# Optimization experiments

Hardware: AMD Instinct MI355X
Metric: run time of the kernel (lower is better)

## Reference

```python
import jax, jax.numpy as jnp
import numpy as np

N_QUBITS = 4
N_LAYERS = 2
BATCH = 524288


def _apply_1q(state, U, axis):
    # state: [B, 2,2,2,2]; U: [2,2] (shared) or [B,2,2] (per-sample); axis = wire index + 1
    s = jnp.moveaxis(state, axis, -1)
    if U.ndim == 3:
        s = jnp.einsum('bij,b...j->b...i', U, s)
    else:
        s = jnp.einsum('ij,...j->...i', U, s)
    return jnp.moveaxis(s, -1, axis)


def _apply_cz(state, a, b):
    # diagonal CZ: flip sign where both qubits are |1>
    sign = jnp.array([[1.0, 1.0], [1.0, -1.0]], dtype=state.dtype)
    shape = [1] * state.ndim
    shape[a] = 2
    shape[b] = 2
    return state * sign.reshape(shape)


def _quantum_expval(feats, w):
    # feats: [B, n_qubits] angles; w: [n_layers, n_qubits, 3] Rot params
    B = feats.shape[0]
    state = jnp.zeros((B,) + (2,) * N_QUBITS, jnp.complex64)
    state = state.at[(slice(None),) + (0,) * N_QUBITS].set(1.0)
    # per-sample RY embedding
    for i in range(N_QUBITS):
        c = jnp.cos(feats[:, i] * 0.5)
        s = jnp.sin(feats[:, i] * 0.5)
        U = jnp.stack([jnp.stack([c, -s], -1), jnp.stack([s, c], -1)], -2).astype(jnp.complex64)
        state = _apply_1q(state, U, i + 1)
    # variational layers: Rot(phi,theta,omega) = RZ(omega) RY(theta) RZ(phi), then CZ chain
    for l in range(N_LAYERS):
        for i in range(N_QUBITS):
            phi, theta, omega = w[l, i, 0], w[l, i, 1], w[l, i, 2]
            ct = jnp.cos(theta * 0.5)
            st = jnp.sin(theta * 0.5)
            U = jnp.stack([
                jnp.stack([jnp.exp(-0.5j * (phi + omega)) * ct, -jnp.exp(0.5j * (phi - omega)) * st]),
                jnp.stack([jnp.exp(-0.5j * (phi - omega)) * st, jnp.exp(0.5j * (phi + omega)) * ct]),
            ]).astype(jnp.complex64)
            state = _apply_1q(state, U, i + 1)
        for i in range(N_QUBITS - 1):
            state = _apply_cz(state, i + 1, i + 2)
    probs = jnp.square(jnp.abs(state))
    p = probs.sum(axis=tuple(range(2, N_QUBITS + 1)))  # marginal of wire 0 -> [B, 2]
    return (p[:, 0] - p[:, 1]).astype(jnp.float32)  # <Z_0>


def setup_inputs() -> dict:
    key = jax.random.key(0)
    ks = jax.random.split(key, 12)
    f = jnp.float32
    return {
        'text': jax.random.normal(ks[0], (BATCH, 16), f),
        'image': jax.random.normal(ks[1], (BATCH, 48), f),
        'tW1': jax.random.normal(ks[2], (16, 32), f) * 0.25,
        'tb1': jnp.zeros((32,), f),
        'tW2': jax.random.normal(ks[3], (32, N_QUBITS), f) * 0.18,
        'tb2': jnp.zeros((N_QUBITS,), f),
        'iW1': jax.random.normal(ks[4], (48, 64), f) * 0.14,
        'ib1': jnp.zeros((64,), f),
        'iW2': jax.random.normal(ks[5], (64, N_QUBITS), f) * 0.125,
        'ib2': jnp.zeros((N_QUBITS,), f),
        'qweights': jax.random.normal(ks[6], (N_LAYERS, N_QUBITS, 3), f),
        'cW1': jax.random.normal(ks[7], (1, 16), f),
        'cb1': jnp.zeros((16,), f),
        'cW2': jax.random.normal(ks[8], (16, 2), f) * 0.25,
        'cb2': jnp.zeros((2,), f),
    }


def reference(text, image, tW1, tb1, tW2, tb2, iW1, ib1, iW2, ib2, qweights, cW1, cb1, cW2, cb2):
    tf = jax.nn.relu(text @ tW1 + tb1) @ tW2 + tb2      # [B, 4]
    imf = jax.nn.relu(image @ iW1 + ib1) @ iW2 + ib2    # [B, 4]
    feats = (tf + imf) * 0.5                             # [B, 4]
    q = _quantum_expval(feats, qweights)                 # [B]
    h = jax.nn.relu(q[:, None] @ cW1 + cb1)              # [B, 16]
    return h @ cW2 + cb2                                 # [B, 2]
```

## Files before the change

kernel.cpp:

```cpp
#include <hip/hip_runtime.h>
#include <math.h>

#define NQ 4
#define NL 2

__global__ void qnn_precompute_A(const float* __restrict__ qw, float* __restrict__ A)
{
    __shared__ float Mre[16][16];
    __shared__ float Mim[16][16];
    int t = threadIdx.x;
    if (t < 16) {
        int j = t;
        float re[16], im[16];
        for (int b = 0; b < 16; ++b) { re[b] = (b == j) ? 1.f : 0.f; im[b] = 0.f; }
        for (int l = 0; l < NL; ++l) {
            for (int i = 0; i < NQ; ++i) {
                float phi   = qw[(l*NQ + i)*3 + 0];
                float theta = qw[(l*NQ + i)*3 + 1];
                float omega = qw[(l*NQ + i)*3 + 2];
                float ct, st; sincosf(0.5f*theta, &st, &ct);
                float ap = 0.5f*(phi + omega);
                float am = 0.5f*(phi - omega);
                float cap, sap, cam, sam;
                sincosf(ap, &sap, &cap);
                sincosf(am, &sam, &cam);
                float u00r =  cap*ct, u00i = -sap*ct;
                float u01r = -cam*st, u01i = -sam*st;
                float u10r =  cam*st, u10i = -sam*st;
                float u11r =  cap*ct, u11i =  sap*ct;
                int mask = 1 << (3 - i);
                for (int b = 0; b < 16; ++b) {
                    if (b & mask) continue;
                    int b1 = b | mask;
                    float a0r = re[b],  a0i = im[b];
                    float a1r = re[b1], a1i = im[b1];
                    re[b]  = u00r*a0r - u00i*a0i + u01r*a1r - u01i*a1i;
                    im[b]  = u00r*a0i + u00i*a0r + u01r*a1i + u01i*a1r;
                    re[b1] = u10r*a0r - u10i*a0i + u11r*a1r - u11i*a1i;
                    im[b1] = u10r*a0i + u10i*a0r + u11r*a1i + u11i*a1r;
                }
            }
            for (int b = 0; b < 16; ++b) {
                float sgn = 1.f;
                if ((b & 0xC) == 0xC) sgn = -sgn;
                if ((b & 0x6) == 0x6) sgn = -sgn;
                if ((b & 0x3) == 0x3) sgn = -sgn;
                re[b] *= sgn; im[b] *= sgn;
            }
        }
        for (int b = 0; b < 16; ++b) { Mre[j][b] = re[b]; Mim[j][b] = im[b]; }
    }
    __syncthreads();
    {
        int j = t >> 4, k = t & 15;
        float s = 0.f;
        #pragma unroll
        for (int b = 0; b < 16; ++b) {
            float sg = (b & 8) ? -1.f : 1.f;
            s += sg * (Mre[j][b]*Mre[k][b] + Mim[j][b]*Mim[k][b]);
        }
        A[j*16 + k] = s;
    }
}

__global__ __launch_bounds__(256, 4) void qnn_main(
    const float* __restrict__ text, const float* __restrict__ image,
    const float* __restrict__ tW1, const float* __restrict__ tb1,
    const float* __restrict__ tW2, const float* __restrict__ tb2,
    const float* __restrict__ iW1, const float* __restrict__ ib1,
    const float* __restrict__ iW2, const float* __restrict__ ib2,
    const float* __restrict__ A,
    const float* __restrict__ cW1, const float* __restrict__ cb1,
    const float* __restrict__ cW2, const float* __restrict__ cb2,
    float* __restrict__ out, int B)
{
    int b = blockIdx.x * blockDim.x + threadIdx.x;
    if (b >= B) return;

    float h2[64];
    #pragma unroll
    for (int j = 0; j < 64; ++j) h2[j] = ib1[j];
    {
        const float4* i4 = (const float4*)(image + (size_t)b * 48);
        #pragma unroll 2
        for (int k4 = 0; k4 < 12; ++k4) {
            float4 v = i4[k4];
            const float* w = iW1 + k4 * 4 * 64;
            #pragma unroll
            for (int j = 0; j < 64; ++j) h2[j] = fmaf(v.x, w[j],       h2[j]);
            #pragma unroll
            for (int j = 0; j < 64; ++j) h2[j] = fmaf(v.y, w[64 + j],  h2[j]);
            #pragma unroll
            for (int j = 0; j < 64; ++j) h2[j] = fmaf(v.z, w[128 + j], h2[j]);
            #pragma unroll
            for (int j = 0; j < 64; ++j) h2[j] = fmaf(v.w, w[192 + j], h2[j]);
        }
    }
    float imf[4];
    #pragma unroll
    for (int o = 0; o < 4; ++o) imf[o] = ib2[o];
    #pragma unroll
    for (int j = 0; j < 64; ++j) {
        float r = fmaxf(h2[j], 0.f);
        const float* w2 = iW2 + j * 4;
        #pragma unroll
        for (int o = 0; o < 4; ++o) imf[o] = fmaf(r, w2[o], imf[o]);
    }

    float h1[32];
    #pragma unroll
    for (int j = 0; j < 32; ++j) h1[j] = tb1[j];
    {
        const float4* t4 = (const float4*)(text + (size_t)b * 16);
        #pragma unroll
        for (int k4 = 0; k4 < 4; ++k4) {
            float4 v = t4[k4];
            const float* w = tW1 + k4 * 4 * 32;
            #pragma unroll
            for (int j = 0; j < 32; ++j) h1[j] = fmaf(v.x, w[j],      h1[j]);
            #pragma unroll
            for (int j = 0; j < 32; ++j) h1[j] = fmaf(v.y, w[32 + j], h1[j]);
            #pragma unroll
            for (int j = 0; j < 32; ++j) h1[j] = fmaf(v.z, w[64 + j], h1[j]);
            #pragma unroll
            for (int j = 0; j < 32; ++j) h1[j] = fmaf(v.w, w[96 + j], h1[j]);
        }
    }
    float tf[4];
    #pragma unroll
    for (int o = 0; o < 4; ++o) tf[o] = tb2[o];
    #pragma unroll
    for (int j = 0; j < 32; ++j) {
        float r = fmaxf(h1[j], 0.f);
        const float* w2 = tW2 + j * 4;
        #pragma unroll
        for (int o = 0; o < 4; ++o) tf[o] = fmaf(r, w2[o], tf[o]);
    }

    float c[4], s[4];
    #pragma unroll
    for (int i = 0; i < 4; ++i) {
        float f = (tf[i] + imf[i]) * 0.25f;
        __sincosf(f, &s[i], &c[i]);
    }
    float p01[4] = { c[0]*c[1], c[0]*s[1], s[0]*c[1], s[0]*s[1] };
    float p23[4] = { c[2]*c[3], c[2]*s[3], s[2]*c[3], s[2]*s[3] };
    float psi[16];
    #pragma unroll
    for (int x = 0; x < 4; ++x)
        #pragma unroll
        for (int y = 0; y < 4; ++y)
            psi[x*4+y] = p01[x] * p23[y];

    float q = 0.f;
    #pragma unroll
    for (int j = 0; j < 16; ++j) {
        float row = 0.f;
        #pragma unroll
        for (int k = 0; k < 16; ++k) row = fmaf(A[j*16+k], psi[k], row);
        q = fmaf(psi[j], row, q);
    }

    float o0 = cb2[0], o1 = cb2[1];
    #pragma unroll
    for (int j = 0; j < 16; ++j) {
        float h = fmaxf(fmaf(q, cW1[j], cb1[j]), 0.f);
        o0 = fmaf(h, cW2[j*2+0], o0);
        o1 = fmaf(h, cW2[j*2+1], o1);
    }
    float2* o2 = (float2*)out;
    o2[b] = make_float2(o0, o1);
}

extern "C" void kernel_launch(void* const* d_in, const int* in_sizes, int n_in,
                              void* d_out, int out_size, void* d_ws, size_t ws_size,
                              hipStream_t stream)
{
    const float* text  = (const float*)d_in[0];
    const float* image = (const float*)d_in[1];
    const float* tW1   = (const float*)d_in[2];
    const float* tb1   = (const float*)d_in[3];
    const float* tW2   = (const float*)d_in[4];
    const float* tb2   = (const float*)d_in[5];
    const float* iW1   = (const float*)d_in[6];
    const float* ib1   = (const float*)d_in[7];
    const float* iW2   = (const float*)d_in[8];
    const float* ib2   = (const float*)d_in[9];
    const float* qw    = (const float*)d_in[10];
    const float* cW1   = (const float*)d_in[11];
    const float* cb1   = (const float*)d_in[12];
    const float* cW2   = (const float*)d_in[13];
    const float* cb2   = (const float*)d_in[14];

    float* A = (float*)d_ws;
    int B = in_sizes[0] / 16;

    qnn_precompute_A<<<1, 256, 0, stream>>>(qw, A);

    int block = 256;
    int grid = (B + block - 1) / block;
    qnn_main<<<grid, block, 0, stream>>>(
        text, image, tW1, tb1, tW2, tb2, iW1, ib1, iW2, ib2,
        A, cW1, cb1, cW2, cb2, (float*)d_out, B);
}
```

Measured before the change: 257.6 us.

## Fuse A precompute into main kernel, stage weights in LDS, 4 samples per thread with packed FMA

Merges the separate A-matrix precompute kernel into one fused kernel in which every block recomputes A and stages all MLP weights in shared memory. Each thread now handles four samples, using 2-wide float vectors so the compiler can emit packed FMA, and the hidden layer is processed in 16-wide chunks to limit register pressure. This reuses each weight read across four samples and removes a kernel launch. In exchange every block pays for weight staging and the redundant A computation, and occupancy changes because of the larger LDS footprint and the new launch bounds.

```diff
diff --git a/kernel.cpp b/kernel.cpp
--- a/kernel.cpp
+++ b/kernel.cpp
@@ -4,31 +4,91 @@
 #define NQ 4
 #define NL 2
 
-__global__ void qnn_precompute_A(const float* __restrict__ qw, float* __restrict__ A)
+typedef float v2f __attribute__((ext_vector_type(2)));
+
+static __device__ __forceinline__ v2f vsplat(float x) { v2f r; r.x = x; r.y = x; return r; }
+static __device__ __forceinline__ v2f vfma(v2f a, float b, v2f c) {
+#if __has_builtin(__builtin_elementwise_fma)
+    return __builtin_elementwise_fma(a, vsplat(b), c);
+#else
+    v2f r; r.x = __builtin_fmaf(a.x, b, c.x); r.y = __builtin_fmaf(a.y, b, c.y); return r;
+#endif
+}
+static __device__ __forceinline__ v2f vfmav(v2f a, v2f b, v2f c) {
+#if __has_builtin(__builtin_elementwise_fma)
+    return __builtin_elementwise_fma(a, b, c);
+#else
+    v2f r; r.x = __builtin_fmaf(a.x, b.x, c.x); r.y = __builtin_fmaf(a.y, b.y, c.y); return r;
+#endif
+}
+static __device__ __forceinline__ v2f vrelu(v2f a) {
+    v2f r; r.x = fmaxf(a.x, 0.f); r.y = fmaxf(a.y, 0.f); return r;
+}
+static __device__ __forceinline__ float fget(float4 v, int k) {
+    return (k == 0) ? v.x : (k == 1) ? v.y : (k == 2) ? v.z : v.w;
+}
+
+#define O_IW1 0
+#define O_IW2 3072
+#define O_TW1 3328
+#define O_TW2 3840
+#define O_IB1 3968
+#define O_TB1 4032
+#define O_FB2 4064
+#define O_CW1 4068
+#define O_CB1 4084
+#define O_CW2 4100
+#define O_CB2 4132
+#define O_AS  4136
+#define O_MRE 4392
+#define O_MIM 4648
+#define LDS_FLOATS 4904
+
+__global__ __launch_bounds__(256, 3) void qnn_fused(
+    const float* __restrict__ text, const float* __restrict__ image,
+    const float* __restrict__ tW1, const float* __restrict__ tb1,
+    const float* __restrict__ tW2, const float* __restrict__ tb2,
+    const float* __restrict__ iW1, const float* __restrict__ ib1,
+    const float* __restrict__ iW2, const float* __restrict__ ib2,
+    const float* __restrict__ qw,
+    const float* __restrict__ cW1, const float* __restrict__ cb1,
+    const float* __restrict__ cW2, const float* __restrict__ cb2,
+    float* __restrict__ out, int B)
 {
-    __shared__ float Mre[16][16];
-    __shared__ float Mim[16][16];
-    int t = threadIdx.x;
-    if (t < 16) {
-        int j = t;
+    __shared__ __align__(16) float W[LDS_FLOATS];
+    const int tid = threadIdx.x;
+
+    for (int i = tid; i < 3072; i += 256) W[O_IW1 + i] = iW1[i];
+    W[O_IW2 + tid] = iW2[tid];
+    for (int i = tid; i < 512; i += 256) W[O_TW1 + i] = tW1[i];
+    if (tid < 128) W[O_TW2 + tid] = tW2[tid];
+    if (tid < 64)  W[O_IB1 + tid] = ib1[tid];
+    if (tid < 32)  W[O_TB1 + tid] = tb1[tid];
+    if (tid < 4)   W[O_FB2 + tid] = ib2[tid] + tb2[tid];
+    if (tid < 16) { W[O_CW1 + tid] = cW1[tid]; W[O_CB1 + tid] = cb1[tid]; }
+    if (tid < 32)  W[O_CW2 + tid] = cW2[tid];
+    if (tid < 2)   W[O_CB2 + tid] = cb2[tid];
+
+    if (tid < 16) {
+        const int j = tid;
         float re[16], im[16];
+        #pragma unroll
         for (int b = 0; b < 16; ++b) { re[b] = (b == j) ? 1.f : 0.f; im[b] = 0.f; }
         for (int l = 0; l < NL; ++l) {
             for (int i = 0; i < NQ; ++i) {
                 float phi   = qw[(l*NQ + i)*3 + 0];
                 float theta = qw[(l*NQ + i)*3 + 1];
                 float omega = qw[(l*NQ + i)*3 + 2];
-                float ct, st; sincosf(0.5f*theta, &st, &ct);
-                float ap = 0.5f*(phi + omega);
-                float am = 0.5f*(phi - omega);
+                float ct, st; __sincosf(0.5f*theta, &st, &ct);
                 float cap, sap, cam, sam;
-                sincosf(ap, &sap, &cap);
-                sincosf(am, &sam, &cam);
+                __sincosf(0.5f*(phi + omega), &sap, &cap);
+                __sincosf(0.5f*(phi - omega), &sam, &cam);
                 float u00r =  cap*ct, u00i = -sap*ct;
                 float u01r = -cam*st, u01i = -sam*st;
                 float u10r =  cam*st, u10i = -sam*st;
                 float u11r =  cap*ct, u11i =  sap*ct;
                 int mask = 1 << (3 - i);
+                #pragma unroll
                 for (int b = 0; b < 16; ++b) {
                     if (b & mask) continue;
                     int b1 = b | mask;
@@ -40,6 +100,7 @@
                     im[b1] = u10r*a0i + u10i*a0r + u11r*a1i + u11i*a1r;
                 }
             }
+            #pragma unroll
             for (int b = 0; b < 16; ++b) {
                 float sgn = 1.f;
                 if ((b & 0xC) == 0xC) sgn = -sgn;
@@ -48,128 +109,175 @@
                 re[b] *= sgn; im[b] *= sgn;
             }
         }
-        for (int b = 0; b < 16; ++b) { Mre[j][b] = re[b]; Mim[j][b] = im[b]; }
+        #pragma unroll
+        for (int b = 0; b < 16; ++b) { W[O_MRE + j*16 + b] = re[b]; W[O_MIM + j*16 + b] = im[b]; }
     }
     __syncthreads();
     {
-        int j = t >> 4, k = t & 15;
-        float s = 0.f;
+        int j = tid >> 4, k = tid & 15;
+        float sacc = 0.f;
         #pragma unroll
         for (int b = 0; b < 16; ++b) {
             float sg = (b & 8) ? -1.f : 1.f;
-            s += sg * (Mre[j][b]*Mre[k][b] + Mim[j][b]*Mim[k][b]);
-        }
-        A[j*16 + k] = s;
-    }
-}
-
-__global__ __launch_bounds__(256, 4) void qnn_main(
-    const float* __restrict__ text, const float* __restrict__ image,
-    const float* __restrict__ tW1, const float* __restrict__ tb1,
-    const float* __restrict__ tW2, const float* __restrict__ tb2,
-    const float* __restrict__ iW1, const float* __restrict__ ib1,
-    const float* __restrict__ iW2, const float* __restrict__ ib2,
-    const float* __restrict__ A,
-    const float* __restrict__ cW1, const float* __restrict__ cb1,
-    const float* __restrict__ cW2, const float* __restrict__ cb2,
-    float* __restrict__ out, int B)
-{
-    int b = blockIdx.x * blockDim.x + threadIdx.x;
-    if (b >= B) return;
-
-    float h2[64];
+            sacc += sg * (W[O_MRE + j*16 + b]*W[O_MRE + k*16 + b] +
+                          W[O_MIM + j*16 + b]*W[O_MIM + k*16 + b]);
+        }
+        W[O_AS + tid] = sacc;
+    }
+    __syncthreads();
+
+    int base = blockIdx.x * 1024 + tid;
+    const int sA = (base       < B) ? base       : B - 1;
+    const int sB = (base + 256 < B) ? base + 256 : B - 1;
+    const int sC = (base + 512 < B) ? base + 512 : B - 1;
+    const int sD = (base + 768 < B) ? base + 768 : B - 1;
+
+    const float4* Wi1 = (const float4*)&W[O_IW1];
+    const float4* Wi2 = (const float4*)&W[O_IW2];
+    const float4* Wt1 = (const float4*)&W[O_TW1];
+    const float4* Wt2 = (const float4*)&W[O_TW2];
+    const float4* As4 = (const float4*)&W[O_AS];
+
+    v2f imf0[4], imf1[4];
     #pragma unroll
-    for (int j = 0; j < 64; ++j) h2[j] = ib1[j];
+    for (int o = 0; o < 4; ++o) { imf0[o] = vsplat(0.f); imf1[o] = vsplat(0.f); }
     {
-        const float4* i4 = (const float4*)(image + (size_t)b * 48);
-        #pragma unroll 2
-        for (int k4 = 0; k4 < 12; ++k4) {
-            float4 v = i4[k4];
-            const float* w = iW1 + k4 * 4 * 64;
-            #pragma unroll
-            for (int j = 0; j < 64; ++j) h2[j] = fmaf(v.x, w[j],       h2[j]);
-            #pragma unroll
-            for (int j = 0; j < 64; ++j) h2[j] = fmaf(v.y, w[64 + j],  h2[j]);
-            #pragma unroll
-            for (int j = 0; j < 64; ++j) h2[j] = fmaf(v.z, w[128 + j], h2[j]);
-            #pragma unroll
-            for (int j = 0; j < 64; ++j) h2[j] = fmaf(v.w, w[192 + j], h2[j]);
-        }
-    }
-    float imf[4];
+        const float4* img4 = (const float4*)image;
+        const size_t rA = (size_t)sA * 12, rB = (size_t)sB * 12;
+        const size_t rC = (size_t)sC * 12, rD = (size_t)sD * 12;
+        for (int q4 = 0; q4 < 4; ++q4) {
+            v2f a0[16], a1[16];
+            #pragma unroll
+            for (int j = 0; j < 16; ++j) {
+                float bv = W[O_IB1 + q4*16 + j];
+                a0[j] = vsplat(bv); a1[j] = vsplat(bv);
+            }
+            #pragma unroll 4
+            for (int k4 = 0; k4 < 12; ++k4) {
+                float4 xA = img4[rA + k4];
+                float4 xB = img4[rB + k4];
+                float4 xC = img4[rC + k4];
+                float4 xD = img4[rD + k4];
+                #pragma unroll
+                for (int kk = 0; kk < 4; ++kk) {
+                    v2f e0; e0.x = fget(xA, kk); e0.y = fget(xB, kk);
+                    v2f e1; e1.x = fget(xC, kk); e1.y = fget(xD, kk);
+                    #pragma unroll
+                    for (int m = 0; m < 4; ++m) {
+                        float4 w = Wi1[(k4*4 + kk)*16 + q4*4 + m];
+                        a0[4*m+0] = vfma(e0, w.x, a0[4*m+0]); a1[4*m+0] = vfma(e1, w.x, a1[4*m+0]);
+                        a0[4*m+1] = vfma(e0, w.y, a0[4*m+1]); a1[4*m+1] = vfma(e1, w.y, a1[4*m+1]);
+                        a0[4*m+2] = vfma(e0, w.z, a0[4*m+2]); a1[4*m+2] = vfma(e1, w.z, a1[4*m+2]);
+                        a0[4*m+3] = vfma(e0, w.w, a0[4*m+3]); a1[4*m+3] = vfma(e1, w.w, a1[4*m+3]);
+                    }
+                }
+            }
+            #pragma unroll
+            for (int j = 0; j < 16; ++j) {
+                float4 w2 = Wi2[q4*16 + j];
+                v2f r0 = vrelu(a0[j]), r1 = vrelu(a1[j]);
+                imf0[0] = vfma(r0, w2.x, imf0[0]); imf1[0] = vfma(r1, w2.x, imf1[0]);
+                imf0[1] = vfma(r0, w2.y, imf0[1]); imf1[1] = vfma(r1, w2.y, imf1[1]);
+                imf0[2] = vfma(r0, w2.z, imf0[2]); imf1[2] = vfma(r1, w2.z, imf1[2]);
+                imf0[3] = vfma(r0, w2.w, imf0[3]); imf1[3] = vfma(r1, w2.w, imf1[3]);
+            }
+        }
+    }
+
+    v2f tf0[4], tf1[4];
     #pragma unroll
-    for (int o = 0; o < 4; ++o) imf[o] = ib2[o];
+    for (int o = 0; o < 4; ++o) { tf0[o] = vsplat(0.f); tf1[o] = vsplat(0.f); }
+    {
+        const float4* txt4 = (const float4*)text;
+        const size_t rA = (size_t)sA * 4, rB = (size_t)sB * 4;
+        const size_t rC = (size_t)sC * 4, rD = (size_t)sD * 4;
+        for (int h2 = 0; h2 < 2; ++h2) {
+            v2f a0[16], a1[16];
+            #pragma unroll
+            for (int j = 0; j < 16; ++j) {
+                float bv = W[O_TB1 + h2*16 + j];
+                a0[j] = vsplat(bv); a1[j] = vsplat(bv);
+            }
+            #pragma unroll
+            for (int k4 = 0; k4 < 4; ++k4) {
+                float4 xA = txt4[rA + k4];
+                float4 xB = txt4[rB + k4];
+                float4 xC = txt4[rC + k4];
+                float4 xD = txt4[rD + k4];
+                #pragma unroll
+                for (int kk = 0; kk < 4; ++kk) {
+                    v2f e0; e0.x = fget(xA, kk); e0.y = fget(xB, kk);
+                    v2f e1; e1.x = fget(xC, kk); e1.y = fget(xD, kk);
+                    #pragma unroll
+                    for (int m = 0; m < 4; ++m) {
+                        float4 w = Wt1[(k4*4 + kk)*8 + h2*4 + m];
+                        a0[4*m+0] = vfma(e0, w.x, a0[4*m+0]); a1[4*m+0] = vfma(e1, w.x, a1[4*m+0]);
+                        a0[4*m+1] = vfma(e0, w.y, a0[4*m+1]); a1[4*m+1] = vfma(e1, w.y, a1[4*m+1]);
+                        a0[4*m+2] = vfma(e0, w.z, a0[4*m+2]); a1[4*m+2] = vfma(e1, w.z, a1[4*m+2]);
+                        a0[4*m+3] = vfma(e0, w.w, a0[4*m+3]); a1[4*m+3] = vfma(e1, w.w, a1[4*m+3]);
+                    }
+                }
+            }
+            #pragma unroll
+            for (int j = 0; j < 16; ++j) {
+                float4 w2 = Wt2[h2*16 + j];
+                v2f r0 = vrelu(a0[j]), r1 = vrelu(a1[j]);
+                tf0[0] = vfma(r0, w2.x, tf0[0]); tf1[0] = vfma(r1, w2.x, tf1[0]);
+                tf0[1] = vfma(r0, w2.y, tf0[1]); tf1[1] = vfma(r1, w2.y, tf1[1]);
+                tf0[2] = vfma(r0, w2.z, tf0[2]); tf1[2] = vfma(r1, w2.z, tf1[2]);
+                tf0[3] = vfma(r0, w2.w, tf0[3]); tf1[3] = vfma(r1, w2.w, tf1[3]);
+            }
+        }
+    }
+
+    float2* o2 = (float2*)out;
     #pragma unroll
-    for (int j = 0; j < 64; ++j) {
-        float r = fmaxf(h2[j], 0.f);
-        const float* w2 = iW2 + j * 4;
-        #pragma unroll
-        for (int o = 0; o < 4; ++o) imf[o] = fmaf(r, w2[o], imf[o]);
-    }
-
-    float h1[32];
-    #pragma unroll
-    for (int j = 0; j < 32; ++j) h1[j] = tb1[j];
-    {
-        const float4* t4 = (const float4*)(text + (size_t)b * 16);
-        #pragma unroll
-        for (int k4 = 0; k4 < 4; ++k4) {
-            float4 v = t4[k4];
-            const float* w = tW1 + k4 * 4 * 32;
-            #pragma unroll
-            for (int j = 0; j < 32; ++j) h1[j] = fmaf(v.x, w[j],      h1[j]);
-            #pragma unroll
-            for (int j = 0; j < 32; ++j) h1[j] = fmaf(v.y, w[32 + j], h1[j]);
-            #pragma unroll
-            for (int j = 0; j < 32; ++j) h1[j] = fmaf(v.z, w[64 + j], h1[j]);
-            #pragma unroll
-            for (int j = 0; j < 32; ++j) h1[j] = fmaf(v.w, w[96 + j], h1[j]);
-        }
-    }
-    float tf[4];
-    #pragma unroll
-    for (int o = 0; o < 4; ++o) tf[o] = tb2[o];
-    #pragma unroll
-    for (int j = 0; j < 32; ++j) {
-        float r = fmaxf(h1[j], 0.f);
-        const float* w2 = tW2 + j * 4;
-        #pragma unroll
-        for (int o = 0; o < 4; ++o) tf[o] = fmaf(r, w2[o], tf[o]);
-    }
-
-    float c[4], s[4];
-    #pragma unroll
-    for (int i = 0; i < 4; ++i) {
-        float f = (tf[i] + imf[i]) * 0.25f;
-        __sincosf(f, &s[i], &c[i]);
-    }
-    float p01[4] = { c[0]*c[1], c[0]*s[1], s[0]*c[1], s[0]*s[1] };
-    float p23[4] = { c[2]*c[3], c[2]*s[3], s[2]*c[3], s[2]*s[3] };
-    float psi[16];
-    #pragma unroll
-    for (int x = 0; x < 4; ++x)
-        #pragma unroll
-        for (int y = 0; y < 4; ++y)
-            psi[x*4+y] = p01[x] * p23[y];
-
-    float q = 0.f;
-    #pragma unroll
-    for (int j = 0; j < 16; ++j) {
-        float row = 0.f;
-        #pragma unroll
-        for (int k = 0; k < 16; ++k) row = fmaf(A[j*16+k], psi[k], row);
-        q = fmaf(psi[j], row, q);
-    }
-
-    float o0 = cb2[0], o1 = cb2[1];
-    #pragma unroll
-    for (int j = 0; j < 16; ++j) {
-        float h = fmaxf(fmaf(q, cW1[j], cb1[j]), 0.f);
-        o0 = fmaf(h, cW2[j*2+0], o0);
-        o1 = fmaf(h, cW2[j*2+1], o1);
-    }
-    float2* o2 = (float2*)out;
-    o2[b] = make_float2(o0, o1);
+    for (int pr = 0; pr < 2; ++pr) {
+        v2f c[4], s[4];
+        #pragma unroll
+        for (int i = 0; i < 4; ++i) {
+            v2f f = ((pr ? imf1[i] : imf0[i]) + (pr ? tf1[i] : tf0[i]) + vsplat(W[O_FB2 + i])) * 0.25f;
+            float sx, cx, sy, cy;
+            __sincosf(f.x, &sx, &cx);
+            __sincosf(f.y, &sy, &cy);
+            c[i].x = cx; c[i].y = cy; s[i].x = sx; s[i].y = sy;
+        }
+        v2f p01[4] = { c[0]*c[1], c[0]*s[1], s[0]*c[1], s[0]*s[1] };
+        v2f p23[4] = { c[2]*c[3], c[2]*s[3], s[2]*c[3], s[2]*s[3] };
+        v2f psi[16];
+        #pragma unroll
+        for (int x = 0; x < 4; ++x)
+            #pragma unroll
+            for (int y = 0; y < 4; ++y)
+                psi[x*4+y] = p01[x] * p23[y];
+
+        v2f q = vsplat(0.f);
+        #pragma unroll
+        for (int j = 0; j < 16; ++j) {
+            v2f row = vsplat(0.f);
+            #pragma unroll
+            for (int k4 = 0; k4 < 4; ++k4) {
+                float4 a = As4[j*4 + k4];
+                row = vfma(psi[k4*4+0], a.x, row);
+                row = vfma(psi[k4*4+1], a.y, row);
+                row = vfma(psi[k4*4+2], a.z, row);
+                row = vfma(psi[k4*4+3], a.w, row);
+            }
+            q = vfmav(psi[j], row, q);
+        }
+
+        v2f o0 = vsplat(W[O_CB2 + 0]), o1v = vsplat(W[O_CB2 + 1]);
+        #pragma unroll
+        for (int j = 0; j < 16; ++j) {
+            float w1 = W[O_CW1 + j], b1 = W[O_CB1 + j];
+            v2f h = vrelu(vfma(q, w1, vsplat(b1)));
+            o0  = vfma(h, W[O_CW2 + j*2 + 0], o0);
+            o1v = vfma(h, W[O_CW2 + j*2 + 1], o1v);
+        }
+        int sX = base + pr*512, sY = sX + 256;
+        if (sX < B) o2[sX] = make_float2(o0.x, o1v.x);
+        if (sY < B) o2[sY] = make_float2(o0.y, o1v.y);
+    }
 }
 
 extern "C" void kernel_launch(void* const* d_in, const int* in_sizes, int n_in,
@@ -192,14 +300,10 @@
     const float* cW2   = (const float*)d_in[13];
     const float* cb2   = (const float*)d_in[14];
 
-    float* A = (float*)d_ws;
     int B = in_sizes[0] / 16;
-
-    qnn_precompute_A<<<1, 256, 0, stream>>>(qw, A);
-
-    int block = 256;
-    int grid = (B + block - 1) / block;
-    qnn_main<<<grid, block, 0, stream>>>(
+    int grid = (B + 1023) / 1024;
+
+    qnn_fused<<<grid, 256, 0, stream>>>(
         text, image, tW1, tb1, tW2, tb2, iW1, ib1, iW2, ib2,
-        A, cW1, cb1, cW2, cb2, (float*)d_out, B);
-}
+        qw, cW1, cb1, cW2, cb2, (float*)d_out, B);
+}
```

Measured after the change: 416.3 us. 61.6% more time.
